# Kernel tuning notes

Hardware: AMD Instinct MI355X
Metric: run time of the kernel (lower is better)

Reference implementation:

```python
import jax, jax.numpy as jnp
import numpy as np

B = 16384
D = 1024          # entity_dim
N_LAYERS = 4
TEMPERATURE = 32.0  # sqrt(entity_dim)


def setup_inputs() -> dict:
    key = jax.random.key(0)
    ks = jax.random.split(key, 6)
    d2 = 2 * D
    scale = 1.0 / np.sqrt(d2)
    x1 = jax.random.normal(ks[0], (B, D), dtype=jnp.float32)
    x2 = jax.random.normal(ks[1], (B, D), dtype=jnp.float32)
    # stacked per-layer Linear(2D, 2D) params; torch Linear stores W as [out, in]
    Ws = jax.random.normal(ks[2], (N_LAYERS, d2, d2), dtype=jnp.float32) * scale
    bs = jax.random.normal(ks[3], (N_LAYERS, d2), dtype=jnp.float32) * scale
    W_last = jax.random.normal(ks[4], (D, d2), dtype=jnp.float32) * scale
    b_last = jax.random.normal(ks[5], (D,), dtype=jnp.float32) * scale
    return {"x1": x1, "x2": x2, "Ws": Ws, "bs": bs, "W_last": W_last, "b_last": b_last}


def reference(x1, x2, Ws, bs, W_last, b_last):
    # x: [B, 2, D]
    x = jnp.stack((x1, x2), axis=1)
    # attn: [B, 2, 2] -- tiny self-attention over the 2 tokens
    attn = jnp.einsum('bsd,btd->bst', x / TEMPERATURE, x)
    attn = jax.nn.softmax(attn, axis=-1)  # dropout = identity in eval mode
    x = jnp.einsum('bst,btd->bsd', attn, x)
    # concat the two attended tokens -> [B, 2D]
    h = jnp.concatenate((x[:, 0, :], x[:, 1, :]), axis=-1)
    for i in range(N_LAYERS):
        h = jax.nn.relu(h @ Ws[i].T + bs[i])
    return h @ W_last.T + b_last
```

## Files before the change

### kernel.cpp

```cpp
#include <hip/hip_runtime.h>

typedef __bf16 bf16x8 __attribute__((ext_vector_type(8)));
typedef float f32x4 __attribute__((ext_vector_type(4)));

__device__ __forceinline__ unsigned short f2bf(float f) {
    unsigned int u = __builtin_bit_cast(unsigned int, f);
    u += 0x7FFFu + ((u >> 16) & 1u);
    return (unsigned short)(u >> 16);
}

__global__ void cvt_kernel(const float* __restrict__ in,
                           unsigned short* __restrict__ out, long n4) {
    long i = (long)blockIdx.x * blockDim.x + threadIdx.x;
    long stride = (long)gridDim.x * blockDim.x;
    for (; i < n4; i += stride) {
        float4 v = ((const float4*)in)[i];
        ushort4 o;
        o.x = f2bf(v.x); o.y = f2bf(v.y); o.z = f2bf(v.z); o.w = f2bf(v.w);
        ((ushort4*)out)[i] = o;
    }
}

__global__ __launch_bounds__(256) void attn_kernel(
    const float* __restrict__ x1, const float* __restrict__ x2,
    unsigned short* __restrict__ h) {
    const int D = 1024;
    const int lane = threadIdx.x & 63;
    const int wave = threadIdx.x >> 6;
    const long row = (long)blockIdx.x * 4 + wave;
    const float4* p1 = (const float4*)(x1 + row * D);
    const float4* p2 = (const float4*)(x2 + row * D);
    float4 v1[4], v2[4];
    float s11 = 0.f, s12 = 0.f, s22 = 0.f;
#pragma unroll
    for (int j = 0; j < 4; ++j) {
        v1[j] = p1[lane + 64 * j];
        v2[j] = p2[lane + 64 * j];
        s11 += v1[j].x * v1[j].x + v1[j].y * v1[j].y + v1[j].z * v1[j].z + v1[j].w * v1[j].w;
        s12 += v1[j].x * v2[j].x + v1[j].y * v2[j].y + v1[j].z * v2[j].z + v1[j].w * v2[j].w;
        s22 += v2[j].x * v2[j].x + v2[j].y * v2[j].y + v2[j].z * v2[j].z + v2[j].w * v2[j].w;
    }
#pragma unroll
    for (int off = 1; off < 64; off <<= 1) {
        s11 += __shfl_xor(s11, off);
        s12 += __shfl_xor(s12, off);
        s22 += __shfl_xor(s22, off);
    }
    const float a00 = 1.f / (1.f + expf((s12 - s11) * (1.f / 32.f)));
    const float a10 = 1.f / (1.f + expf((s22 - s12) * (1.f / 32.f)));
    const float a01 = 1.f - a00, a11 = 1.f - a10;
    unsigned short* h0 = h + row * 2048;
#pragma unroll
    for (int j = 0; j < 4; ++j) {
        const int f = lane + 64 * j;
        ushort4 o0, o1;
        o0.x = f2bf(a00 * v1[j].x + a01 * v2[j].x);
        o0.y = f2bf(a00 * v1[j].y + a01 * v2[j].y);
        o0.z = f2bf(a00 * v1[j].z + a01 * v2[j].z);
        o0.w = f2bf(a00 * v1[j].w + a01 * v2[j].w);
        o1.x = f2bf(a10 * v1[j].x + a11 * v2[j].x);
        o1.y = f2bf(a10 * v1[j].y + a11 * v2[j].y);
        o1.z = f2bf(a10 * v1[j].z + a11 * v2[j].z);
        o1.w = f2bf(a10 * v1[j].w + a11 * v2[j].w);
        ((ushort4*)(h0))[f] = o0;
        ((ushort4*)(h0 + 1024))[f] = o1;
    }
}

#define BAR   __builtin_amdgcn_s_barrier()
#define LGKM0 do { asm volatile("s_waitcnt lgkmcnt(0)" ::: "memory"); \
                   __builtin_amdgcn_sched_barrier(0); } while (0)
#define VMW(n) asm volatile("s_waitcnt vmcnt(" #n ")" ::: "memory")

#define MMQ(mb)                                                                \
  _Pragma("unroll") for (int n = 0; n < 4; ++n)                                \
  _Pragma("unroll") for (int mq = 0; mq < 4; ++mq)                             \
    acc[(mb) + mq][n] = __builtin_amdgcn_mfma_f32_16x16x32_bf16(               \
        Bf[n], Af[mq], acc[(mb) + mq][n], 0, 0, 0);

template <bool RELU, typename OT>
__global__ __launch_bounds__(512, 2) void gemm256(
    const unsigned short* __restrict__ A,
    const unsigned short* __restrict__ Bw,
    const float* __restrict__ bias,
    OT* __restrict__ C,
    int N, int K) {
    __shared__ __align__(16) unsigned short lds[65536];
    const int tid = threadIdx.x;
    const int lane = tid & 63, wave = tid >> 6;
    const int wm = wave >> 2, wn = wave & 3;
    const int fr = lane & 15, fq = lane >> 4;

    const int nbn = N >> 8;
    const int sh = (nbn == 8) ? 3 : 2;
    const int cpx = (int)gridDim.x >> 3;
    const int swz = ((int)blockIdx.x & 7) * cpx + ((int)blockIdx.x >> 3);
    const int bn = swz & (nbn - 1);
    const int bm = swz >> sh;
    const long m0 = (long)bm * 256, n0 = (long)bn * 256;
    const long rowb = (long)K * 2;

    const int flip = ((fr >> 3) & 1) << 5;
    const int lbase = fr * 64 + ((fq * 16) ^ flip);
    const int aRd = wm * 8192 + lbase;
    const int bRd = 32768 + wn * 4096 + lbase;
    const char* ldsc = (const char*)lds;

    const int srow = wave * 16 + (lane >> 2);
    const int scol = ((lane & 3) << 4) ^ ((lane >> 5) << 5);
    const char* Abl = (const char*)A + m0 * rowb;
    const char* Bbl = (const char*)Bw + n0 * rowb;

    auto stage = [&](const char* mb, int regbase, int kh, int kt) {
#pragma unroll
        for (int L = 0; L < 2; ++L) {
            const int r = L * 128 + srow;
            const char* src = mb + (long)r * rowb + kt * 128 + kh * 64 + scol;
            __builtin_amdgcn_global_load_lds(
                (const __attribute__((address_space(1))) void*)src,
                (__attribute__((address_space(3))) void*)((char*)lds +
                    (regbase + kh * 16384 + L * 8192 + wave * 1024)),
                16, 0, 0);
        }
    };

    f32x4 acc[8][4] = {};
    bf16x8 Bf[4], Af[4];

    auto rdB = [&](int Tb, int kh) {
        const int b = Tb + kh * 16384 + bRd;
#pragma unroll
        for (int nf = 0; nf < 4; ++nf)
            Bf[nf] = *(const bf16x8*)(ldsc + b + nf * 1024);
    };
    auto rdA = [&](int Tb, int kh, int mh) {
        const int b = Tb + kh * 16384 + aRd + mh * 4096;
#pragma unroll
        for (int mq = 0; mq < 4; ++mq)
            Af[mq] = *(const bf16x8*)(ldsc + b + mq * 1024);
    };

    stage(Bbl, 32768, 0, 0);
    stage(Abl, 0,     0, 0);
    stage(Bbl, 32768, 1, 0);
    stage(Abl, 0,     1, 0);
    stage(Bbl, 65536 + 32768, 0, 1);
    stage(Abl, 65536,         0, 1);
    VMW(8);
    BAR;

    const int NT = K >> 6, NIT = NT >> 1;
    for (int i = 0; i < NIT - 1; ++i) {
        const int u = 2 * i + 1, t2 = 2 * i + 2, t3 = 2 * i + 3;
        stage(Bbl, 65536 + 32768, 1, u);
        rdB(0, 0); rdA(0, 0, 0);
        VMW(8); BAR; LGKM0; MMQ(0);
        stage(Abl, 65536, 1, u);
        rdA(0, 0, 1);
        VMW(8); BAR; LGKM0; MMQ(4);
        stage(Bbl, 32768, 0, t2);
        rdB(0, 1); rdA(0, 1, 0);
        VMW(8); BAR; LGKM0; MMQ(0);
        stage(Abl, 0, 0, t2);
        rdA(0, 1, 1);
        VMW(8); BAR; LGKM0; MMQ(4);
        stage(Bbl, 32768, 1, t2);
        rdB(65536, 0); rdA(65536, 0, 0);
        VMW(8); BAR; LGKM0; MMQ(0);
        stage(Abl, 0, 1, t2);
        rdA(65536, 0, 1);
        VMW(8); BAR; LGKM0; MMQ(4);
        stage(Bbl, 65536 + 32768, 0, t3);
        rdB(65536, 1); rdA(65536, 1, 0);
        VMW(8); BAR; LGKM0; MMQ(0);
        stage(Abl, 65536, 0, t3);
        rdA(65536, 1, 1);
        VMW(8); BAR; LGKM0; MMQ(4);
    }
    {
        const int u = NT - 1;
        stage(Bbl, 65536 + 32768, 1, u);
        rdB(0, 0); rdA(0, 0, 0);
        VMW(8); BAR; LGKM0; MMQ(0);
        stage(Abl, 65536, 1, u);
        rdA(0, 0, 1);
        VMW(8); BAR; LGKM0; MMQ(4);
        rdB(0, 1); rdA(0, 1, 0);
        VMW(8); BAR; LGKM0; MMQ(0);
        rdA(0, 1, 1);
        VMW(4); BAR; LGKM0; MMQ(4);
        rdB(65536, 0); rdA(65536, 0, 0);
        VMW(4); BAR; LGKM0; MMQ(0);
        rdA(65536, 0, 1);
        VMW(0); BAR; LGKM0; MMQ(4);
        rdB(65536, 1); rdA(65536, 1, 0);
        VMW(0); BAR; LGKM0; MMQ(0);
        rdA(65536, 1, 1);
        VMW(0); BAR; LGKM0; MMQ(4);
    }

    const long crow0 = m0 + wm * 128 + fr;
    const long ccol0 = n0 + wn * 64 + fq * 4;
    float4 bv[4];
#pragma unroll
    for (int n = 0; n < 4; ++n) bv[n] = *(const float4*)(bias + ccol0 + n * 16);
#pragma unroll
    for (int m = 0; m < 8; ++m) {
        const long rb = (crow0 + m * 16) * N;
#pragma unroll
        for (int n = 0; n < 4; ++n) {
            float v0 = acc[m][n][0] + bv[n].x;
            float v1 = acc[m][n][1] + bv[n].y;
            float v2 = acc[m][n][2] + bv[n].z;
            float v3 = acc[m][n][3] + bv[n].w;
            if (RELU) {
                v0 = v0 > 0.f ? v0 : 0.f; v1 = v1 > 0.f ? v1 : 0.f;
                v2 = v2 > 0.f ? v2 : 0.f; v3 = v3 > 0.f ? v3 : 0.f;
            }
            if constexpr (sizeof(OT) == 2) {
                uint2 oo;
                oo.x = (unsigned)f2bf(v0) | ((unsigned)f2bf(v1) << 16);
                oo.y = (unsigned)f2bf(v2) | ((unsigned)f2bf(v3) << 16);
                *(uint2*)((unsigned short*)C + rb + ccol0 + n * 16) = oo;
            } else {
                *(float4*)((float*)C + rb + ccol0 + n * 16) =
                    make_float4(v0, v1, v2, v3);
            }
        }
    }
}

extern "C" void kernel_launch(void* const* d_in, const int* in_sizes, int n_in,
                              void* d_out, int out_size, void* d_ws, size_t ws_size,
                              hipStream_t stream) {
    const float* x1 = (const float*)d_in[0];
    const float* x2 = (const float*)d_in[1];
    const float* Ws = (const float*)d_in[2];
    const float* bs = (const float*)d_in[3];
    const float* Wl = (const float*)d_in[4];
    const float* bl = (const float*)d_in[5];
    float* out = (float*)d_out;

    char* ws = (char*)d_ws;
    unsigned short* hA  = (unsigned short*)(ws);
    unsigned short* hB  = (unsigned short*)(ws + (67108864L));
    unsigned short* Wbf = (unsigned short*)(ws + (134217728L));
    unsigned short* Wlb = (unsigned short*)(ws + (167772160L));

    cvt_kernel<<<2048, 256, 0, stream>>>(Ws, Wbf, 4L * 2048 * 2048 / 4);
    cvt_kernel<<<512, 256, 0, stream>>>(Wl, Wlb, 1024L * 2048 / 4);

    attn_kernel<<<16384 / 4, 256, 0, stream>>>(x1, x2, hA);

    gemm256<true, unsigned short><<<512, 512, 0, stream>>>(hA, Wbf + 0L * 2048 * 2048, bs + 0 * 2048, hB, 2048, 2048);
    gemm256<true, unsigned short><<<512, 512, 0, stream>>>(hB, Wbf + 1L * 2048 * 2048, bs + 1 * 2048, hA, 2048, 2048);
    gemm256<true, unsigned short><<<512, 512, 0, stream>>>(hA, Wbf + 2L * 2048 * 2048, bs + 2 * 2048, hB, 2048, 2048);
    gemm256<true, unsigned short><<<512, 512, 0, stream>>>(hB, Wbf + 3L * 2048 * 2048, bs + 3 * 2048, hA, 2048, 2048);
    gemm256<false, float><<<256, 512, 0, stream>>>(hA, Wlb, bl, out, 1024, 2048);
}
```

Before: 597.9 us.

## Double-buffer LDS fragment registers to overlap LDS reads with MFMA

Replaces the single A/B fragment register set with two ping-pong sets so the LDS reads for the next sub-step are issued before the current MFMA block runs. The explicit lgkmcnt(0) wait and sched barrier are removed, and vmcnt thresholds are retuned to the new order. Launch bounds drop from 2 to 1 block per CU to give room for the extra fragment registers. The cost is lower occupancy and a risk of read-after-write hazards on the shared buffers if the barrier placement no longer covers every reuse.

```diff
diff --git a/kernel.cpp b/kernel.cpp
--- a/kernel.cpp
+++ b/kernel.cpp
@@ -68,18 +68,16 @@
 }
 
 #define BAR   __builtin_amdgcn_s_barrier()
-#define LGKM0 do { asm volatile("s_waitcnt lgkmcnt(0)" ::: "memory"); \
-                   __builtin_amdgcn_sched_barrier(0); } while (0)
 #define VMW(n) asm volatile("s_waitcnt vmcnt(" #n ")" ::: "memory")
 
-#define MMQ(mb)                                                                \
+#define MMQ(mb, BS, AS)                                                        \
   _Pragma("unroll") for (int n = 0; n < 4; ++n)                                \
   _Pragma("unroll") for (int mq = 0; mq < 4; ++mq)                             \
     acc[(mb) + mq][n] = __builtin_amdgcn_mfma_f32_16x16x32_bf16(               \
-        Bf[n], Af[mq], acc[(mb) + mq][n], 0, 0, 0);
+        BS[n], AS[mq], acc[(mb) + mq][n], 0, 0, 0);
 
 template <bool RELU, typename OT>
-__global__ __launch_bounds__(512, 2) void gemm256(
+__global__ __launch_bounds__(512, 1) void gemm256(
     const unsigned short* __restrict__ A,
     const unsigned short* __restrict__ Bw,
     const float* __restrict__ bias,
@@ -125,19 +123,19 @@
     };
 
     f32x4 acc[8][4] = {};
-    bf16x8 Bf[4], Af[4];
-
-    auto rdB = [&](int Tb, int kh) {
+    bf16x8 Bf0[4], Bf1[4], Af0[4], Af1[4];
+
+    auto rdB = [&](int Tb, int kh, bf16x8 (&D)[4]) {
         const int b = Tb + kh * 16384 + bRd;
 #pragma unroll
         for (int nf = 0; nf < 4; ++nf)
-            Bf[nf] = *(const bf16x8*)(ldsc + b + nf * 1024);
+            D[nf] = *(const bf16x8*)(ldsc + b + nf * 1024);
     };
-    auto rdA = [&](int Tb, int kh, int mh) {
+    auto rdA = [&](int Tb, int kh, int mh, bf16x8 (&D)[4]) {
         const int b = Tb + kh * 16384 + aRd + mh * 4096;
 #pragma unroll
         for (int mq = 0; mq < 4; ++mq)
-            Af[mq] = *(const bf16x8*)(ldsc + b + mq * 1024);
+            D[mq] = *(const bf16x8*)(ldsc + b + mq * 1024);
     };
 
     stage(Bbl, 32768, 0, 0);
@@ -148,55 +146,70 @@
     stage(Abl, 65536,         0, 1);
     VMW(8);
     BAR;
+    rdB(0, 0, Bf0); rdA(0, 0, 0, Af0);
 
     const int NT = K >> 6, NIT = NT >> 1;
     for (int i = 0; i < NIT - 1; ++i) {
         const int u = 2 * i + 1, t2 = 2 * i + 2, t3 = 2 * i + 3;
         stage(Bbl, 65536 + 32768, 1, u);
-        rdB(0, 0); rdA(0, 0, 0);
-        VMW(8); BAR; LGKM0; MMQ(0);
+        rdA(0, 0, 1, Af1);
+        MMQ(0, Bf0, Af0);
+        VMW(6); BAR;
         stage(Abl, 65536, 1, u);
-        rdA(0, 0, 1);
-        VMW(8); BAR; LGKM0; MMQ(4);
+        rdB(0, 1, Bf1); rdA(0, 1, 0, Af0);
+        MMQ(4, Bf0, Af1);
+        VMW(6); BAR;
         stage(Bbl, 32768, 0, t2);
-        rdB(0, 1); rdA(0, 1, 0);
-        VMW(8); BAR; LGKM0; MMQ(0);
+        rdA(0, 1, 1, Af1);
+        MMQ(0, Bf1, Af0);
+        VMW(6); BAR;
         stage(Abl, 0, 0, t2);
-        rdA(0, 1, 1);
-        VMW(8); BAR; LGKM0; MMQ(4);
+        rdB(65536, 0, Bf0); rdA(65536, 0, 0, Af0);
+        MMQ(4, Bf1, Af1);
+        VMW(6); BAR;
         stage(Bbl, 32768, 1, t2);
-        rdB(65536, 0); rdA(65536, 0, 0);
-        VMW(8); BAR; LGKM0; MMQ(0);
+        rdA(65536, 0, 1, Af1);
+        MMQ(0, Bf0, Af0);
+        VMW(6); BAR;
         stage(Abl, 0, 1, t2);
-        rdA(65536, 0, 1);
-        VMW(8); BAR; LGKM0; MMQ(4);
+        rdB(65536, 1, Bf1); rdA(65536, 1, 0, Af0);
+        MMQ(4, Bf0, Af1);
+        VMW(6); BAR;
         stage(Bbl, 65536 + 32768, 0, t3);
-        rdB(65536, 1); rdA(65536, 1, 0);
-        VMW(8); BAR; LGKM0; MMQ(0);
+        rdA(65536, 1, 1, Af1);
+        MMQ(0, Bf1, Af0);
+        VMW(6); BAR;
         stage(Abl, 65536, 0, t3);
-        rdA(65536, 1, 1);
-        VMW(8); BAR; LGKM0; MMQ(4);
+        rdB(0, 0, Bf0); rdA(0, 0, 0, Af0);
+        MMQ(4, Bf1, Af1);
+        VMW(6); BAR;
     }
     {
         const int u = NT - 1;
         stage(Bbl, 65536 + 32768, 1, u);
-        rdB(0, 0); rdA(0, 0, 0);
-        VMW(8); BAR; LGKM0; MMQ(0);
+        rdA(0, 0, 1, Af1);
+        MMQ(0, Bf0, Af0);
+        VMW(6); BAR;
         stage(Abl, 65536, 1, u);
-        rdA(0, 0, 1);
-        VMW(8); BAR; LGKM0; MMQ(4);
-        rdB(0, 1); rdA(0, 1, 0);
-        VMW(8); BAR; LGKM0; MMQ(0);
-        rdA(0, 1, 1);
-        VMW(4); BAR; LGKM0; MMQ(4);
-        rdB(65536, 0); rdA(65536, 0, 0);
-        VMW(4); BAR; LGKM0; MMQ(0);
-        rdA(65536, 0, 1);
-        VMW(0); BAR; LGKM0; MMQ(4);
-        rdB(65536, 1); rdA(65536, 1, 0);
-        VMW(0); BAR; LGKM0; MMQ(0);
-        rdA(65536, 1, 1);
-        VMW(0); BAR; LGKM0; MMQ(4);
+        rdB(0, 1, Bf1); rdA(0, 1, 0, Af0);
+        MMQ(4, Bf0, Af1);
+        VMW(6); BAR;
+        rdA(0, 1, 1, Af1);
+        MMQ(0, Bf1, Af0);
+        VMW(4); BAR;
+        rdB(65536, 0, Bf0); rdA(65536, 0, 0, Af0);
+        MMQ(4, Bf1, Af1);
+        VMW(2); BAR;
+        rdA(65536, 0, 1, Af1);
+        MMQ(0, Bf0, Af0);
+        VMW(0); BAR;
+        rdB(65536, 1, Bf1); rdA(65536, 1, 0, Af0);
+        MMQ(4, Bf0, Af1);
+        BAR;
+        rdA(65536, 1, 1, Af1);
+        MMQ(0, Bf1, Af0);
+        BAR;
+        MMQ(4, Bf1, Af1);
     }
 
     const long crow0 = m0 + wm * 128 + fr;
```

After: 606.4 us. No clear change (+1.4%).

## Merge GEMM K-loop phases and double-buffer A fragments in registers

Applied to the files above, without the earlier changes.

Restructures the main GEMM loop from eight barrier-separated phases into four. Each phase now stages both B and A halves, reads B plus both A fragment halves into separate register sets (Af0/Af1), then runs 32 MFMAs back to back, with a trailing barrier protecting LDS reuse. The explicit lgkmcnt(0) wait and sched_barrier are removed, so the compiler can interleave LDS reads with MFMAs. The intent is to cut per-MFMA-group synchronisation overhead and enlarge the issue window, at the cost of extra fragment registers, which may cause spills under the 512x2 launch bounds.

```diff
diff --git a/kernel.cpp b/kernel.cpp
--- a/kernel.cpp
+++ b/kernel.cpp
@@ -68,15 +68,13 @@
 }
 
 #define BAR   __builtin_amdgcn_s_barrier()
-#define LGKM0 do { asm volatile("s_waitcnt lgkmcnt(0)" ::: "memory"); \
-                   __builtin_amdgcn_sched_barrier(0); } while (0)
 #define VMW(n) asm volatile("s_waitcnt vmcnt(" #n ")" ::: "memory")
 
-#define MMQ(mb)                                                                \
+#define MMQ(mb, AS)                                                            \
   _Pragma("unroll") for (int n = 0; n < 4; ++n)                                \
   _Pragma("unroll") for (int mq = 0; mq < 4; ++mq)                             \
     acc[(mb) + mq][n] = __builtin_amdgcn_mfma_f32_16x16x32_bf16(               \
-        Bf[n], Af[mq], acc[(mb) + mq][n], 0, 0, 0);
+        Bf[n], AS[mq], acc[(mb) + mq][n], 0, 0, 0);
 
 template <bool RELU, typename OT>
 __global__ __launch_bounds__(512, 2) void gemm256(
@@ -125,7 +123,7 @@
     };
 
     f32x4 acc[8][4] = {};
-    bf16x8 Bf[4], Af[4];
+    bf16x8 Bf[4], Af0[4], Af1[4];
 
     auto rdB = [&](int Tb, int kh) {
         const int b = Tb + kh * 16384 + bRd;
@@ -133,11 +131,11 @@
         for (int nf = 0; nf < 4; ++nf)
             Bf[nf] = *(const bf16x8*)(ldsc + b + nf * 1024);
     };
-    auto rdA = [&](int Tb, int kh, int mh) {
+    auto rdA = [&](int Tb, int kh, int mh, bf16x8 (&D)[4]) {
         const int b = Tb + kh * 16384 + aRd + mh * 4096;
 #pragma unroll
         for (int mq = 0; mq < 4; ++mq)
-            Af[mq] = *(const bf16x8*)(ldsc + b + mq * 1024);
+            D[mq] = *(const bf16x8*)(ldsc + b + mq * 1024);
     };
 
     stage(Bbl, 32768, 0, 0);
@@ -152,51 +150,45 @@
     const int NT = K >> 6, NIT = NT >> 1;
     for (int i = 0; i < NIT - 1; ++i) {
         const int u = 2 * i + 1, t2 = 2 * i + 2, t3 = 2 * i + 3;
-        stage(Bbl, 65536 + 32768, 1, u);
-        rdB(0, 0); rdA(0, 0, 0);
-        VMW(8); BAR; LGKM0; MMQ(0);
-        stage(Abl, 65536, 1, u);
-        rdA(0, 0, 1);
-        VMW(8); BAR; LGKM0; MMQ(4);
-        stage(Bbl, 32768, 0, t2);
-        rdB(0, 1); rdA(0, 1, 0);
-        VMW(8); BAR; LGKM0; MMQ(0);
-        stage(Abl, 0, 0, t2);
-        rdA(0, 1, 1);
-        VMW(8); BAR; LGKM0; MMQ(4);
-        stage(Bbl, 32768, 1, t2);
-        rdB(65536, 0); rdA(65536, 0, 0);
-        VMW(8); BAR; LGKM0; MMQ(0);
-        stage(Abl, 0, 1, t2);
-        rdA(65536, 0, 1);
-        VMW(8); BAR; LGKM0; MMQ(4);
-        stage(Bbl, 65536 + 32768, 0, t3);
-        rdB(65536, 1); rdA(65536, 1, 0);
-        VMW(8); BAR; LGKM0; MMQ(0);
-        stage(Abl, 65536, 0, t3);
-        rdA(65536, 1, 1);
-        VMW(8); BAR; LGKM0; MMQ(4);
+        stage(Bbl, 65536 + 32768, 1, u); stage(Abl, 65536, 1, u);
+        rdB(0, 0); rdA(0, 0, 0, Af0); rdA(0, 0, 1, Af1);
+        VMW(8); BAR;
+        MMQ(0, Af0); MMQ(4, Af1);
+        BAR;
+        stage(Bbl, 32768, 0, t2); stage(Abl, 0, 0, t2);
+        rdB(0, 1); rdA(0, 1, 0, Af0); rdA(0, 1, 1, Af1);
+        VMW(8); BAR;
+        MMQ(0, Af0); MMQ(4, Af1);
+        BAR;
+        stage(Bbl, 32768, 1, t2); stage(Abl, 0, 1, t2);
+        rdB(65536, 0); rdA(65536, 0, 0, Af0); rdA(65536, 0, 1, Af1);
+        VMW(8); BAR;
+        MMQ(0, Af0); MMQ(4, Af1);
+        BAR;
+        stage(Bbl, 65536 + 32768, 0, t3); stage(Abl, 65536, 0, t3);
+        rdB(65536, 1); rdA(65536, 1, 0, Af0); rdA(65536, 1, 1, Af1);
+        VMW(8); BAR;
+        MMQ(0, Af0); MMQ(4, Af1);
+        BAR;
     }
     {
         const int u = NT - 1;
-        stage(Bbl, 65536 + 32768, 1, u);
-        rdB(0, 0); rdA(0, 0, 0);
-        VMW(8); BAR; LGKM0; MMQ(0);
-        stage(Abl, 65536, 1, u);
-        rdA(0, 0, 1);
-        VMW(8); BAR; LGKM0; MMQ(4);
-        rdB(0, 1); rdA(0, 1, 0);
-        VMW(8); BAR; LGKM0; MMQ(0);
-        rdA(0, 1, 1);
-        VMW(4); BAR; LGKM0; MMQ(4);
-        rdB(65536, 0); rdA(65536, 0, 0);
-        VMW(4); BAR; LGKM0; MMQ(0);
-        rdA(65536, 0, 1);
-        VMW(0); BAR; LGKM0; MMQ(4);
-        rdB(65536, 1); rdA(65536, 1, 0);
-        VMW(0); BAR; LGKM0; MMQ(0);
-        rdA(65536, 1, 1);
-        VMW(0); BAR; LGKM0; MMQ(4);
+        stage(Bbl, 65536 + 32768, 1, u); stage(Abl, 65536, 1, u);
+        rdB(0, 0); rdA(0, 0, 0, Af0); rdA(0, 0, 1, Af1);
+        VMW(8); BAR;
+        MMQ(0, Af0); MMQ(4, Af1);
+        BAR;
+        rdB(0, 1); rdA(0, 1, 0, Af0); rdA(0, 1, 1, Af1);
+        VMW(4); BAR;
+        MMQ(0, Af0); MMQ(4, Af1);
+        BAR;
+        rdB(65536, 0); rdA(65536, 0, 0, Af0); rdA(65536, 0, 1, Af1);
+        VMW(0); BAR;
+        MMQ(0, Af0); MMQ(4, Af1);
+        BAR;
+        rdB(65536, 1); rdA(65536, 1, 0, Af0); rdA(65536, 1, 1, Af1);
+        BAR;
+        MMQ(0, Af0); MMQ(4, Af1);
     }
 
     const long crow0 = m0 + wm * 128 + fr;
```

Measured after the change: 614.6 us. +2.8%, slower.
